# Kernel tuning notes

Measured on AMD Instinct MI355X. Metric: run time of the kernel, lower is better.

## Reference

```python
import jax, jax.numpy as jnp
import numpy as np

EPS = 1e-3  # tfa GroupNormalization default epsilon


def setup_inputs() -> dict:
    key = jax.random.key(0)
    ks = jax.random.split(key, 6)
    B, H, W, C = 8, 64, 64, 256
    x = jax.random.normal(ks[0], (B, H, W, C), dtype=jnp.float32)
    s = 0.05  # keep activations in a numerically sane range
    return {
        "x": x,
        "gamma": jnp.ones((C,), jnp.float32),
        "beta": jnp.zeros((C,), jnp.float32),
        "wq": jax.random.normal(ks[1], (C, C), jnp.float32) * s,
        "bq": jnp.zeros((C,), jnp.float32),
        "wk": jax.random.normal(ks[2], (C, C), jnp.float32) * s,
        "bk": jnp.zeros((C,), jnp.float32),
        "wv": jax.random.normal(ks[3], (C, C), jnp.float32) * s,
        "bv": jnp.zeros((C,), jnp.float32),
        "wp": jax.random.normal(ks[4], (C, C), jnp.float32) * s,
        "bp": jnp.zeros((C,), jnp.float32),
    }


def _group_norm1(x, gamma, beta):
    # GroupNorm with 1 group: normalize over (H, W, C) per sample,
    # per-channel affine. tfa default epsilon=1e-3.
    mean = jnp.mean(x, axis=(1, 2, 3), keepdims=True)
    var = jnp.var(x, axis=(1, 2, 3), keepdims=True)
    return (x - mean) * jax.lax.rsqrt(var + EPS) * gamma + beta


def reference(x, gamma, beta, wq, bq, wk, bk, wv, bv, wp, bp):
    B, H, W, C = x.shape
    h = _group_norm1(x, gamma, beta)
    hf = h.reshape(B, H * W, C)  # flatten spatial -> tokens
    q = hf @ wq + bq
    k = hf @ wk + bk
    v = hf @ wv + bv
    scale = jnp.float32(C) ** -0.5
    # full [B, N, N] attention scores, N = H*W (faithful to the einsum)
    scores = jnp.einsum('bnc,bmc->bnm', q, k) * scale
    attn = jax.nn.softmax(scores, axis=-1)
    o = jnp.einsum('bnm,bmc->bnc', attn, v)
    o = o @ wp + bp
    return x + o.reshape(B, H, W, C)
```

## Files before the change

kernel.cpp:

```cpp
#include <hip/hip_runtime.h>
#include <hip/hip_bf16.h>

typedef __attribute__((ext_vector_type(8))) short short8;
typedef __attribute__((ext_vector_type(4))) float f32x4;
typedef __attribute__((ext_vector_type(16))) float f32x16;
typedef long long ll_t;

#define WS_PART 0u
#define WS_STATS 4096u
#define WS_WT 8192u
#define WS_ML 532480u
#define WS_Q  2097152u
#define WS_K  (WS_Q + 16777216u)
#define WS_V  (WS_K + 16777216u)
#define WS_VT (WS_V + 16777216u)
#define WS_O  (WS_VT + 16777216u)

__device__ __forceinline__ unsigned short f2bf(float f) {
  unsigned int u = __builtin_bit_cast(unsigned int, f);
  u += 0x7fffu + ((u >> 16) & 1u);
  return (unsigned short)(u >> 16);
}
__device__ __forceinline__ float bf2f(unsigned short h) {
  unsigned int u = ((unsigned int)h) << 16;
  return __builtin_bit_cast(float, u);
}
__device__ __forceinline__ unsigned char f2fp8(float f) {
  return (unsigned char)(__builtin_amdgcn_cvt_pk_fp8_f32(f, f, 0, false) & 0xff);
}

__device__ __forceinline__ void gl_lds16(const unsigned short* g, unsigned short* l) {
  __builtin_amdgcn_global_load_lds(
      (const __attribute__((address_space(1))) unsigned int*)g,
      (__attribute__((address_space(3))) unsigned int*)l, 16, 0, 0);
}

__device__ __forceinline__ f32x4 mfma_fp8(ll_t a, ll_t b, f32x4 c) {
  return __builtin_amdgcn_mfma_f32_16x16x32_fp8_fp8(a, b, c, 0, 0, 0);
}

__global__ void k_wt(const float* __restrict__ wq, const float* __restrict__ wk,
                     const float* __restrict__ wv, const float* __restrict__ wp,
                     unsigned short* __restrict__ wT) {
  int m = blockIdx.x >> 8;
  int c = blockIdx.x & 255;
  const float* w = (m == 0) ? wq : (m == 1) ? wk : (m == 2) ? wv : wp;
  int d = threadIdx.x;
  wT[(size_t)(m * 256 + d) * 256 + c] = f2bf(w[c * 256 + d]);
}

__global__ void k_gn_part(const float* __restrict__ x, float2* __restrict__ part) {
  int b = blockIdx.x >> 5, seg = blockIdx.x & 31;
  const float4* xp = (const float4*)(x + ((size_t)b << 20) + ((size_t)seg << 15));
  float s = 0.f, sq = 0.f;
  for (int i = 0; i < 32; ++i) {
    float4 v = xp[threadIdx.x + i * 256];
    s += v.x + v.y + v.z + v.w;
    sq += v.x * v.x + v.y * v.y + v.z * v.z + v.w * v.w;
  }
  for (int m = 1; m <= 32; m <<= 1) { s += __shfl_xor(s, m); sq += __shfl_xor(sq, m); }
  __shared__ float2 red[4];
  int w = threadIdx.x >> 6;
  if ((threadIdx.x & 63) == 0) red[w] = make_float2(s, sq);
  __syncthreads();
  if (threadIdx.x == 0) {
    float S = 0.f, Q = 0.f;
    for (int i = 0; i < 4; ++i) { S += red[i].x; Q += red[i].y; }
    part[blockIdx.x] = make_float2(S, Q);
  }
}

__global__ void k_gn_stats(const float2* __restrict__ part, float2* __restrict__ stats) {
  int b = blockIdx.x, t = threadIdx.x;
  float s = 0.f, sq = 0.f;
  if (t < 32) { float2 p = part[b * 32 + t]; s = p.x; sq = p.y; }
  for (int m = 1; m <= 32; m <<= 1) { s += __shfl_xor(s, m); sq += __shfl_xor(sq, m); }
  if (t == 0) {
    float mean = s * (1.f / 1048576.f);
    float var = sq * (1.f / 1048576.f) - mean * mean;
    stats[b] = make_float2(mean, rsqrtf(var + 1e-3f));
  }
}

__global__ __launch_bounds__(256) void k_qkv(
    const float* __restrict__ x, const float* __restrict__ gamma, const float* __restrict__ beta,
    const float* __restrict__ bq, const float* __restrict__ bk, const float* __restrict__ bv,
    const float2* __restrict__ stats, const unsigned short* __restrict__ wT,
    unsigned char* __restrict__ q8, unsigned char* __restrict__ k8,
    unsigned char* __restrict__ vt8)
{
  __shared__ unsigned short SMEM[16384];
  unsigned short* const As = SMEM;
  unsigned short* const Bs = SMEM + 8192;
  const int bm = blockIdx.x, bn = blockIdx.y;
  const int mat = bn >> 1, dbase = (bn & 1) * 128;
  const int tid = threadIdx.x, lane = tid & 63, w = tid >> 6;
  const int wm = w >> 1, wn = w & 1;
  const int m0 = bm * 128;
  const float2 st = stats[bm >> 5];
  f32x16 acc[2][2] = {};
  for (int ks = 0; ks < 4; ++ks) {
    for (int i = 0; i < 8; ++i) {
      int chunk = tid + i * 256;
      int row = chunk >> 4, cq = (chunk & 15) * 4;
      int c = ks * 64 + cq;
      const float4 xv = *(const float4*)(x + (size_t)(m0 + row) * 256 + c);
      const float4 g = *(const float4*)(gamma + c);
      const float4 bt = *(const float4*)(beta + c);
      unsigned short h[4];
      h[0] = f2bf((xv.x - st.x) * st.y * g.x + bt.x);
      h[1] = f2bf((xv.y - st.x) * st.y * g.y + bt.y);
      h[2] = f2bf((xv.z - st.x) * st.y * g.z + bt.z);
      h[3] = f2bf((xv.w - st.x) * st.y * g.w + bt.w);
      *(uint2*)(&As[row * 64 + (cq ^ ((row & 7) << 3))]) = *(uint2*)h;
    }
    for (int i = 0; i < 4; ++i) {
      int chunk = tid + i * 256;
      int row = chunk >> 3, cc = (chunk & 7) * 8;
      const uint4* src = (const uint4*)(wT + (size_t)(mat * 256 + dbase + row) * 256 + ks * 64 + cc);
      *(uint4*)(&Bs[row * 64 + (cc ^ ((row & 7) << 3))]) = *src;
    }
    __syncthreads();
    for (int kk = 0; kk < 4; ++kk) {
      short8 a[2], b[2];
      for (int mi = 0; mi < 2; ++mi) {
        int row = wm * 64 + mi * 32 + (lane & 31);
        int off = (kk * 16 + (lane >> 5) * 8) ^ ((row & 7) << 3);
        a[mi] = *(const short8*)(&As[row * 64 + off]);
      }
      for (int ni = 0; ni < 2; ++ni) {
        int row = wn * 64 + ni * 32 + (lane & 31);
        int off = (kk * 16 + (lane >> 5) * 8) ^ ((row & 7) << 3);
        b[ni] = *(const short8*)(&Bs[row * 64 + off]);
      }
      for (int mi = 0; mi < 2; ++mi)
        for (int ni = 0; ni < 2; ++ni)
          acc[mi][ni] = __builtin_amdgcn_mfma_f32_32x32x16_bf16(a[mi], b[ni], acc[mi][ni], 0, 0, 0);
    }
    __syncthreads();
  }
  const int batch = bm >> 5;
  if (mat == 0) {
    for (int ni = 0; ni < 2; ++ni) {
      int dcol = dbase + wn * 64 + ni * 32 + (lane & 31);
      float bv_ = bq[dcol];
      for (int mi = 0; mi < 2; ++mi)
        for (int r = 0; r < 16; ++r) {
          int rowD = (r & 3) + 8 * (r >> 2) + 4 * (lane >> 5);
          int token = m0 + wm * 64 + mi * 32 + rowD;
          q8[(size_t)token * 256 + dcol] = f2fp8((acc[mi][ni][r] + bv_) * 0.25f);
        }
    }
  } else if (mat == 1) {
    for (int ni = 0; ni < 2; ++ni) {
      int dcol = dbase + wn * 64 + ni * 32 + (lane & 31);
      float bv_ = bk[dcol];
      size_t cbase = (size_t)(batch * 32 + (dcol >> 3)) * 32768 + (dcol & 7);
      for (int mi = 0; mi < 2; ++mi)
        for (int r = 0; r < 16; ++r) {
          int rowD = (r & 3) + 8 * (r >> 2) + 4 * (lane >> 5);
          int token = (m0 + wm * 64 + mi * 32 + rowD) & 4095;
          k8[cbase + (size_t)token * 8] = f2fp8((acc[mi][ni][r] + bv_) * 0.25f);
        }
    }
  } else {
    unsigned char* SB = (unsigned char*)SMEM;
    for (int ni = 0; ni < 2; ++ni) {
      int dloc = wn * 64 + ni * 32 + (lane & 31);
      float bv_ = bv[dbase + dloc];
      for (int mi = 0; mi < 2; ++mi)
        for (int r = 0; r < 16; ++r) {
          int tloc = wm * 64 + mi * 32 + (r & 3) + 8 * (r >> 2) + 4 * (lane >> 5);
          SB[dloc * 128 + (tloc ^ ((dloc & 7) << 4))] = f2fp8(acc[mi][ni][r] + bv_);
        }
    }
    __syncthreads();
    const int Tbase = (bm & 31) * 16;
    for (int i2 = 0; i2 < 4; ++i2) {
      int u = tid + i2 * 256;
      int T = u >> 6;
      int dp = u & 63;
      int d0 = dp * 2;
      int tb = T * 8;
      uint2 lo = *(const uint2*)(&SB[d0 * 128 + (tb ^ ((d0 & 7) << 4))]);
      uint2 hi2 = *(const uint2*)(&SB[(d0 + 1) * 128 + (tb ^ (((d0 + 1) & 7) << 4))]);
      uint4 vv = { lo.x, lo.y, hi2.x, hi2.y };
      *(uint4*)(vt8 + ((size_t)(batch * 512 + Tbase + T) * 256 + dbase + d0) * 8) = vv;
    }
  }
}

__global__ __launch_bounds__(512, 2) void k_attn(
    const unsigned char* __restrict__ q8, const unsigned char* __restrict__ k8,
    const unsigned char* __restrict__ vt8,
    unsigned short* __restrict__ part0, unsigned short* __restrict__ part1,
    float2* __restrict__ ml)
{
  __shared__ unsigned char LDSb[131072];
  unsigned char* const Ks0 = LDSb;
  unsigned char* const Ks1 = LDSb + 16384;
  unsigned char* const Vt0 = LDSb + 32768;
  unsigned char* const Vt1 = LDSb + 49152;
  const int g = blockIdx.x & 15, qt = blockIdx.x >> 4;
  const int batch = g >> 1, half = g & 1;
  const int q0 = qt * 256;
  const int tid = threadIdx.x, lane = tid & 63, li = lane & 15, hi = lane >> 4, w = tid >> 6;
  const float L2E = 1.44269504f;

  ll_t qf8[2][8];
#pragma unroll
  for (int qs = 0; qs < 2; ++qs) {
    const size_t qtok = (size_t)(batch * 4096 + q0 + w * 32 + qs * 16 + li);
#pragma unroll
    for (int kt = 0; kt < 8; ++kt)
      qf8[qs][kt] = *(const ll_t*)(q8 + qtok * 256 + kt * 32 + hi * 8);
  }
  f32x4 acc[2][16] = {};
  float m_r[2] = {-INFINITY, -INFINITY};
  float l_r[2] = {0.f, 0.f};
  const int idx0 = ((((hi << 1) + 0) & 3) * 16 + li) << 2;
  const int idx1 = ((((hi << 1) + 1) & 3) * 16 + li) << 2;

  unsigned kSrc[2];
  int kDst[2], vOff[2];
#pragma unroll
  for (int i = 0; i < 2; ++i) {
    kSrc[i] = (unsigned)((w * 4 + 2 * i + (lane >> 5)) * 32768 + (lane & 31) * 16);
    kDst[i] = (w * 4 + 2 * i) * 512 + lane * 16;
    vOff[i] = w * 2048 + i * 1024 + lane * 16;
  }
  const unsigned char* kb = k8 + (size_t)batch * 1048576 + half * 16384;
  const unsigned char* vb = vt8 + (size_t)batch * 1048576 + half * 524288;

#define STAGE(KD, VD) do {                                              \
    _Pragma("unroll")                                                   \
    for (int i = 0; i < 2; ++i)                                         \
      gl_lds16((const unsigned short*)(kb + kSrc[i]),                   \
               (unsigned short*)(KD + kDst[i]));                        \
    _Pragma("unroll")                                                   \
    for (int i = 0; i < 2; ++i)                                         \
      gl_lds16((const unsigned short*)(vb + vOff[i]),                   \
               (unsigned short*)(VD + vOff[i]));                        \
  } while (0)

#define QK(KVF, SDST, KC) do {                                               \
    _Pragma("unroll")                                                        \
    for (int ct = 0; ct < 2; ++ct)                                           \
      _Pragma("unroll")                                                      \
      for (int kt = 0; kt < 8; ++kt) {                                       \
        int boff = (((kt * 4 + hi) * 64) + (KVF) * 32 + ct * 16 + li) * 8;   \
        ll_t kf = *(const ll_t*)(&KC[boff]);                                 \
        SDST[0][ct] = mfma_fp8(kf, qf8[0][kt], SDST[0][ct]);                 \
        SDST[1][ct] = mfma_fp8(kf, qf8[1][kt], SDST[1][ct]);                 \
      }                                                                      \
  } while (0)

#define SOFTMAX(SARR, PF) do {                                               \
    float pm[2];                                                             \
    _Pragma("unroll")                                                        \
    for (int qs = 0; qs < 2; ++qs) {                                         \
      float p = fmaxf(fmaxf(fmaxf(SARR[qs][0][0], SARR[qs][0][1]),           \
                            fmaxf(SARR[qs][0][2], SARR[qs][0][3])),          \
                      fmaxf(fmaxf(SARR[qs][1][0], SARR[qs][1][1]),           \
                            fmaxf(SARR[qs][1][2], SARR[qs][1][3])));         \
      p = fmaxf(p, __shfl_xor(p, 16));                                       \
      p = fmaxf(p, __shfl_xor(p, 32));                                       \
      pm[qs] = p;                                                            \
    }                                                                        \
    if (!__all(fmaxf(pm[0] - m_r[0], pm[1] - m_r[1]) <= 4.0f)) {             \
      _Pragma("unroll")                                                      \
      for (int qs = 0; qs < 2; ++qs) {                                       \
        float mn = fmaxf(m_r[qs], pm[qs]);                                   \
        float corr = exp2f((m_r[qs] - mn) * L2E);                            \
        m_r[qs] = mn;                                                        \
        l_r[qs] *= corr;                                                     \
        float cq[4];                                                         \
        _Pragma("unroll")                                                    \
        for (int r = 0; r < 4; ++r) cq[r] = __shfl(corr, hi * 4 + r);        \
        _Pragma("unroll")                                                    \
        for (int dt = 0; dt < 16; ++dt)                                      \
          _Pragma("unroll")                                                  \
          for (int r = 0; r < 4; ++r) acc[qs][dt][r] *= cq[r];               \
      }                                                                      \
    }                                                                        \
    _Pragma("unroll")                                                        \
    for (int qs = 0; qs < 2; ++qs) {                                         \
      float rs = 0.f;                                                        \
      _Pragma("unroll")                                                      \
      for (int ct = 0; ct < 2; ++ct)                                         \
        _Pragma("unroll")                                                    \
        for (int r = 0; r < 4; ++r) {                                        \
          float p = exp2f((SARR[qs][ct][r] - m_r[qs]) * L2E);                \
          SARR[qs][ct][r] = p;                                               \
          rs += p;                                                           \
        }                                                                    \
      rs += __shfl_xor(rs, 16);                                              \
      rs += __shfl_xor(rs, 32);                                              \
      l_r[qs] += rs;                                                         \
      int D0 = __builtin_amdgcn_cvt_pk_fp8_f32(SARR[qs][0][0], SARR[qs][0][1], 0, false); \
      D0 = __builtin_amdgcn_cvt_pk_fp8_f32(SARR[qs][0][2], SARR[qs][0][3], D0, true);     \
      int D1 = __builtin_amdgcn_cvt_pk_fp8_f32(SARR[qs][1][0], SARR[qs][1][1], 0, false); \
      D1 = __builtin_amdgcn_cvt_pk_fp8_f32(SARR[qs][1][2], SARR[qs][1][3], D1, true);     \
      int a0 = __builtin_amdgcn_ds_bpermute(idx0, D0);                       \
      int a1 = __builtin_amdgcn_ds_bpermute(idx0, D1);                       \
      int b0 = __builtin_amdgcn_ds_bpermute(idx1, D0);                       \
      int b1 = __builtin_amdgcn_ds_bpermute(idx1, D1);                       \
      bool sel = (lane & 32) != 0;                                           \
      int2 pw = { sel ? a1 : a0, sel ? b1 : b0 };                            \
      PF[qs] = __builtin_bit_cast(ll_t, pw);                                 \
    }                                                                        \
  } while (0)

#define PV(KVF, PF, VC) do {                                                 \
    __builtin_amdgcn_s_setprio(1);                                          \
    _Pragma("unroll")                                                        \
    for (int dt = 0; dt < 16; ++dt) {                                        \
      int boff = ((((KVF) * 4 + hi) * 256) + dt * 16 + li) * 8;              \
      ll_t vf = *(const ll_t*)(&VC[boff]);                                   \
      acc[0][dt] = mfma_fp8(PF[0], vf, acc[0][dt]);                          \
      acc[1][dt] = mfma_fp8(PF[1], vf, acc[1][dt]);                          \
    }                                                                        \
    __builtin_amdgcn_s_setprio(0);                                          \
  } while (0)

  STAGE(Ks0, Vt0);
  for (int it = 0; it < 32; ++it) {
    const int cur = it & 1;
    __syncthreads();
    if (it < 31) {
      kb += 512;
      vb += 16384;
      if (cur) STAGE(Ks0, Vt0); else STAGE(Ks1, Vt1);
    }
    const unsigned char* Kc = cur ? Ks1 : Ks0;
    const unsigned char* Vc = cur ? Vt1 : Vt0;

    f32x4 s0[2][2] = {};
    __builtin_amdgcn_s_setprio(1);
    QK(0, s0, Kc);
    __builtin_amdgcn_s_setprio(0);
    ll_t pf0[2];
    SOFTMAX(s0, pf0);

    f32x4 s1[2][2] = {};
    __builtin_amdgcn_s_setprio(1);
    QK(1, s1, Kc);
    __builtin_amdgcn_s_setprio(0);
    PV(0, pf0, Vc);
    ll_t pf1[2];
    SOFTMAX(s1, pf1);
    PV(1, pf1, Vc);
  }
#undef STAGE
#undef QK
#undef SOFTMAX
#undef PV
  __syncthreads();
  if (lane < 16) {
#pragma unroll
    for (int qs = 0; qs < 2; ++qs)
      ml[half * 32768 + (size_t)batch * 4096 + q0 + w * 32 + qs * 16 + lane] =
          make_float2(m_r[qs], l_r[qs]);
  }
  unsigned short* Lw = (unsigned short*)LDSb + w * 8192;
#pragma unroll
  for (int qs = 0; qs < 2; ++qs)
#pragma unroll
    for (int dt = 0; dt < 16; ++dt)
#pragma unroll
      for (int r = 0; r < 4; ++r)
        Lw[(qs * 16 + hi * 4 + r) * 256 + dt * 16 + li] = f2bf(acc[qs][dt][r]);
  unsigned short* pout = (half ? part1 : part0) + ((size_t)batch * 4096 + q0 + w * 32) * 256;
#pragma unroll
  for (int i = 0; i < 16; ++i) {
    short8 v = *(const short8*)(&Lw[i * 512 + lane * 8]);
    int row = i * 2 + (lane >> 5);
    *(short8*)(pout + row * 256 + (lane & 31) * 8) = v;
  }
}

__global__ __launch_bounds__(256) void k_proj(
    const unsigned short* __restrict__ p0, const unsigned short* __restrict__ p1,
    const float2* __restrict__ ml, const unsigned short* __restrict__ wT,
    const float* __restrict__ bp, const float* __restrict__ x, float* __restrict__ out)
{
  __shared__ unsigned short As[128 * 64];
  __shared__ unsigned short Bs[128 * 64];
  const int bm = blockIdx.x, bn = blockIdx.y;
  const int dbase = bn * 128;
  const int tid = threadIdx.x, lane = tid & 63, w = tid >> 6;
  const int wm = w >> 1, wn = w & 1;
  const int m0 = bm * 128;
  f32x16 acc[2][2] = {};
  for (int ks = 0; ks < 4; ++ks) {
    for (int i = 0; i < 4; ++i) {
      int chunk = tid + i * 256;
      int row = chunk >> 3, cc = (chunk & 7) * 8;
      int tok = m0 + row;
      float2 a = ml[tok];
      float2 b2 = ml[32768 + tok];
      float mm = fmaxf(a.x, b2.x);
      float s0 = exp2f((a.x - mm) * 1.44269504f), s1 = exp2f((b2.x - mm) * 1.44269504f);
      float inv = 1.f / (s0 * a.y + s1 * b2.y);
      float r0 = s0 * inv, r1 = s1 * inv;
      short8 u0 = *(const short8*)(p0 + (size_t)tok * 256 + ks * 64 + cc);
      short8 u1 = *(const short8*)(p1 + (size_t)tok * 256 + ks * 64 + cc);
      unsigned short hh[8];
      for (int j = 0; j < 8; ++j)
        hh[j] = f2bf(r0 * bf2f((unsigned short)u0[j]) + r1 * bf2f((unsigned short)u1[j]));
      *(uint4*)(&As[row * 64 + (cc ^ ((row & 7) << 3))]) = *(uint4*)hh;
    }
    for (int i = 0; i < 4; ++i) {
      int chunk = tid + i * 256;
      int row = chunk >> 3, cc = (chunk & 7) * 8;
      const uint4* src = (const uint4*)(wT + (size_t)(3 * 256 + dbase + row) * 256 + ks * 64 + cc);
      *(uint4*)(&Bs[row * 64 + (cc ^ ((row & 7) << 3))]) = *src;
    }
    __syncthreads();
    for (int kk = 0; kk < 4; ++kk) {
      short8 a[2], b[2];
      for (int mi = 0; mi < 2; ++mi) {
        int row = wm * 64 + mi * 32 + (lane & 31);
        int off = (kk * 16 + (lane >> 5) * 8) ^ ((row & 7) << 3);
        a[mi] = *(const short8*)(&As[row * 64 + off]);
      }
      for (int ni = 0; ni < 2; ++ni) {
        int row = wn * 64 + ni * 32 + (lane & 31);
        int off = (kk * 16 + (lane >> 5) * 8) ^ ((row & 7) << 3);
        b[ni] = *(const short8*)(&Bs[row * 64 + off]);
      }
      for (int mi = 0; mi < 2; ++mi)
        for (int ni = 0; ni < 2; ++ni)
          acc[mi][ni] = __builtin_amdgcn_mfma_f32_32x32x16_bf16(a[mi], b[ni], acc[mi][ni], 0, 0, 0);
    }
    __syncthreads();
  }
  for (int ni = 0; ni < 2; ++ni) {
    int dcol = dbase + wn * 64 + ni * 32 + (lane & 31);
    float bv_ = bp[dcol];
    for (int mi = 0; mi < 2; ++mi)
      for (int r = 0; r < 16; ++r) {
        int rowD = (r & 3) + 8 * (r >> 2) + 4 * (lane >> 5);
        size_t idx = (size_t)(m0 + wm * 64 + mi * 32 + rowD) * 256 + dcol;
        out[idx] = x[idx] + acc[mi][ni][r] + bv_;
      }
  }
}

extern "C" void kernel_launch(void* const* d_in, const int* in_sizes, int n_in,
                              void* d_out, int out_size, void* d_ws, size_t ws_size,
                              hipStream_t stream) {
  const float* x = (const float*)d_in[0];
  const float* gamma = (const float*)d_in[1];
  const float* beta = (const float*)d_in[2];
  const float* wq = (const float*)d_in[3];
  const float* bq = (const float*)d_in[4];
  const float* wk = (const float*)d_in[5];
  const float* bk = (const float*)d_in[6];
  const float* wv = (const float*)d_in[7];
  const float* bv = (const float*)d_in[8];
  const float* wp = (const float*)d_in[9];
  const float* bp = (const float*)d_in[10];
  char* ws = (char*)d_ws;
  float2* part = (float2*)(ws + WS_PART);
  float2* stats = (float2*)(ws + WS_STATS);
  unsigned short* wT = (unsigned short*)(ws + WS_WT);
  float2* mlw = (float2*)(ws + WS_ML);
  unsigned char* q8 = (unsigned char*)(ws + WS_Q);
  unsigned char* k8 = (unsigned char*)(ws + WS_K);
  unsigned short* vw = (unsigned short*)(ws + WS_V);
  unsigned char* vt8 = (unsigned char*)(ws + WS_VT);
  unsigned short* ow = (unsigned short*)(ws + WS_O);
  float* out = (float*)d_out;

  k_wt<<<1024, 256, 0, stream>>>(wq, wk, wv, wp, wT);
  k_gn_part<<<256, 256, 0, stream>>>(x, part);
  k_gn_stats<<<8, 64, 0, stream>>>(part, stats);
  k_qkv<<<dim3(256, 6), 256, 0, stream>>>(x, gamma, beta, bq, bk, bv, stats, wT, q8, k8, vt8);
  k_attn<<<256, 512, 0, stream>>>(q8, k8, vt8, vw, ow, mlw);
  k_proj<<<dim3(256, 2), 256, 0, stream>>>(vw, ow, mlw, wT, bp, x, out);
}
```

Measured before the change: 205.3 us.

## Halve attention query tile per wave to double grid and raise occupancy

Each wave of the attention kernel now processes 16 query rows instead of 32. The grid doubles to 512 blocks and the LDS buffer shrinks to 64KB. The launch bound asks for 4 blocks per CU instead of 2, aiming for more resident waves and less register pressure. The cost is that every K/V tile staged into LDS now serves only half as many queries, so K/V global and LDS traffic per unit of work doubles. QK and PV are also serialized within each half-tile, which removes the previous overlap of PV(0) with QK(1).

Result: no change. 201.4 us (-1.9%).

```diff
diff --git a/kernel.cpp b/kernel.cpp
--- a/kernel.cpp
+++ b/kernel.cpp
@@ -190,34 +190,32 @@
   }
 }
 
-__global__ __launch_bounds__(512, 2) void k_attn(
+__global__ __launch_bounds__(512, 4) void k_attn(
     const unsigned char* __restrict__ q8, const unsigned char* __restrict__ k8,
     const unsigned char* __restrict__ vt8,
     unsigned short* __restrict__ part0, unsigned short* __restrict__ part1,
     float2* __restrict__ ml)
 {
-  __shared__ unsigned char LDSb[131072];
+  __shared__ unsigned char LDSb[65536];
   unsigned char* const Ks0 = LDSb;
   unsigned char* const Ks1 = LDSb + 16384;
   unsigned char* const Vt0 = LDSb + 32768;
   unsigned char* const Vt1 = LDSb + 49152;
   const int g = blockIdx.x & 15, qt = blockIdx.x >> 4;
   const int batch = g >> 1, half = g & 1;
-  const int q0 = qt * 256;
+  const int q0 = qt * 128;
   const int tid = threadIdx.x, lane = tid & 63, li = lane & 15, hi = lane >> 4, w = tid >> 6;
   const float L2E = 1.44269504f;
 
-  ll_t qf8[2][8];
-#pragma unroll
-  for (int qs = 0; qs < 2; ++qs) {
-    const size_t qtok = (size_t)(batch * 4096 + q0 + w * 32 + qs * 16 + li);
+  ll_t qf8[8];
+  {
+    const size_t qtok = (size_t)(batch * 4096 + q0 + w * 16 + li);
 #pragma unroll
     for (int kt = 0; kt < 8; ++kt)
-      qf8[qs][kt] = *(const ll_t*)(q8 + qtok * 256 + kt * 32 + hi * 8);
-  }
-  f32x4 acc[2][16] = {};
-  float m_r[2] = {-INFINITY, -INFINITY};
-  float l_r[2] = {0.f, 0.f};
+      qf8[kt] = *(const ll_t*)(q8 + qtok * 256 + kt * 32 + hi * 8);
+  }
+  f32x4 acc[16] = {};
+  float m_r = -INFINITY, l_r = 0.f;
   const int idx0 = ((((hi << 1) + 0) & 3) * 16 + li) << 2;
   const int idx1 = ((((hi << 1) + 1) & 3) * 16 + li) << 2;
 
@@ -250,65 +248,53 @@
       for (int kt = 0; kt < 8; ++kt) {                                       \
         int boff = (((kt * 4 + hi) * 64) + (KVF) * 32 + ct * 16 + li) * 8;   \
         ll_t kf = *(const ll_t*)(&KC[boff]);                                 \
-        SDST[0][ct] = mfma_fp8(kf, qf8[0][kt], SDST[0][ct]);                 \
-        SDST[1][ct] = mfma_fp8(kf, qf8[1][kt], SDST[1][ct]);                 \
+        SDST[ct] = mfma_fp8(kf, qf8[kt], SDST[ct]);                          \
       }                                                                      \
   } while (0)
 
 #define SOFTMAX(SARR, PF) do {                                               \
-    float pm[2];                                                             \
+    float pm = fmaxf(fmaxf(fmaxf(SARR[0][0], SARR[0][1]),                    \
+                           fmaxf(SARR[0][2], SARR[0][3])),                   \
+                     fmaxf(fmaxf(SARR[1][0], SARR[1][1]),                    \
+                           fmaxf(SARR[1][2], SARR[1][3])));                  \
+    pm = fmaxf(pm, __shfl_xor(pm, 16));                                      \
+    pm = fmaxf(pm, __shfl_xor(pm, 32));                                      \
+    if (!__all(pm - m_r <= 4.0f)) {                                          \
+      float mn = fmaxf(m_r, pm);                                             \
+      float corr = exp2f((m_r - mn) * L2E);                                  \
+      m_r = mn;                                                              \
+      l_r *= corr;                                                           \
+      float cq[4];                                                           \
+      _Pragma("unroll")                                                      \
+      for (int r = 0; r < 4; ++r) cq[r] = __shfl(corr, hi * 4 + r);          \
+      _Pragma("unroll")                                                      \
+      for (int dt = 0; dt < 16; ++dt)                                        \
+        _Pragma("unroll")                                                    \
+        for (int r = 0; r < 4; ++r) acc[dt][r] *= cq[r];                     \
+    }                                                                        \
+    float rs = 0.f;                                                          \
     _Pragma("unroll")                                                        \
-    for (int qs = 0; qs < 2; ++qs) {                                         \
-      float p = fmaxf(fmaxf(fmaxf(SARR[qs][0][0], SARR[qs][0][1]),           \
-                            fmaxf(SARR[qs][0][2], SARR[qs][0][3])),          \
-                      fmaxf(fmaxf(SARR[qs][1][0], SARR[qs][1][1]),           \
-                            fmaxf(SARR[qs][1][2], SARR[qs][1][3])));         \
-      p = fmaxf(p, __shfl_xor(p, 16));                                       \
-      p = fmaxf(p, __shfl_xor(p, 32));                                       \
-      pm[qs] = p;                                                            \
-    }                                                                        \
-    if (!__all(fmaxf(pm[0] - m_r[0], pm[1] - m_r[1]) <= 4.0f)) {             \
+    for (int ct = 0; ct < 2; ++ct)                                           \
       _Pragma("unroll")                                                      \
-      for (int qs = 0; qs < 2; ++qs) {                                       \
-        float mn = fmaxf(m_r[qs], pm[qs]);                                   \
-        float corr = exp2f((m_r[qs] - mn) * L2E);                            \
-        m_r[qs] = mn;                                                        \
-        l_r[qs] *= corr;                                                     \
-        float cq[4];                                                         \
-        _Pragma("unroll")                                                    \
-        for (int r = 0; r < 4; ++r) cq[r] = __shfl(corr, hi * 4 + r);        \
-        _Pragma("unroll")                                                    \
-        for (int dt = 0; dt < 16; ++dt)                                      \
-          _Pragma("unroll")                                                  \
-          for (int r = 0; r < 4; ++r) acc[qs][dt][r] *= cq[r];               \
+      for (int r = 0; r < 4; ++r) {                                          \
+        float p = exp2f((SARR[ct][r] - m_r) * L2E);                          \
+        SARR[ct][r] = p;                                                     \
+        rs += p;                                                             \
       }                                                                      \
-    }                                                                        \
-    _Pragma("unroll")                                                        \
-    for (int qs = 0; qs < 2; ++qs) {                                         \
-      float rs = 0.f;                                                        \
-      _Pragma("unroll")                                                      \
-      for (int ct = 0; ct < 2; ++ct)                                         \
-        _Pragma("unroll")                                                    \
-        for (int r = 0; r < 4; ++r) {                                        \
-          float p = exp2f((SARR[qs][ct][r] - m_r[qs]) * L2E);                \
-          SARR[qs][ct][r] = p;                                               \
-          rs += p;                                                           \
-        }                                                                    \
-      rs += __shfl_xor(rs, 16);                                              \
-      rs += __shfl_xor(rs, 32);                                              \
-      l_r[qs] += rs;                                                         \
-      int D0 = __builtin_amdgcn_cvt_pk_fp8_f32(SARR[qs][0][0], SARR[qs][0][1], 0, false); \
-      D0 = __builtin_amdgcn_cvt_pk_fp8_f32(SARR[qs][0][2], SARR[qs][0][3], D0, true);     \
-      int D1 = __builtin_amdgcn_cvt_pk_fp8_f32(SARR[qs][1][0], SARR[qs][1][1], 0, false); \
-      D1 = __builtin_amdgcn_cvt_pk_fp8_f32(SARR[qs][1][2], SARR[qs][1][3], D1, true);     \
-      int a0 = __builtin_amdgcn_ds_bpermute(idx0, D0);                       \
-      int a1 = __builtin_amdgcn_ds_bpermute(idx0, D1);                       \
-      int b0 = __builtin_amdgcn_ds_bpermute(idx1, D0);                       \
-      int b1 = __builtin_amdgcn_ds_bpermute(idx1, D1);                       \
-      bool sel = (lane & 32) != 0;                                           \
-      int2 pw = { sel ? a1 : a0, sel ? b1 : b0 };                            \
-      PF[qs] = __builtin_bit_cast(ll_t, pw);                                 \
-    }                                                                        \
+    rs += __shfl_xor(rs, 16);                                                \
+    rs += __shfl_xor(rs, 32);                                                \
+    l_r += rs;                                                               \
+    int D0 = __builtin_amdgcn_cvt_pk_fp8_f32(SARR[0][0], SARR[0][1], 0, false); \
+    D0 = __builtin_amdgcn_cvt_pk_fp8_f32(SARR[0][2], SARR[0][3], D0, true);     \
+    int D1 = __builtin_amdgcn_cvt_pk_fp8_f32(SARR[1][0], SARR[1][1], 0, false); \
+    D1 = __builtin_amdgcn_cvt_pk_fp8_f32(SARR[1][2], SARR[1][3], D1, true);     \
+    int a0 = __builtin_amdgcn_ds_bpermute(idx0, D0);                         \
+    int a1 = __builtin_amdgcn_ds_bpermute(idx0, D1);                         \
+    int b0 = __builtin_amdgcn_ds_bpermute(idx1, D0);                         \
+    int b1 = __builtin_amdgcn_ds_bpermute(idx1, D1);                         \
+    bool sel = (lane & 32) != 0;                                             \
+    int2 pw = { sel ? a1 : a0, sel ? b1 : b0 };                              \
+    PF = __builtin_bit_cast(ll_t, pw);                                       \
   } while (0)
 
 #define PV(KVF, PF, VC) do {                                                 \
@@ -317,8 +303,7 @@
     for (int dt = 0; dt < 16; ++dt) {                                        \
       int boff = ((((KVF) * 4 + hi) * 256) + dt * 16 + li) * 8;              \
       ll_t vf = *(const ll_t*)(&VC[boff]);                                   \
-      acc[0][dt] = mfma_fp8(PF[0], vf, acc[0][dt]);                          \
-      acc[1][dt] = mfma_fp8(PF[1], vf, acc[1][dt]);                          \
+      acc[dt] = mfma_fp8(PF, vf, acc[dt]);                                   \
     }                                                                        \
     __builtin_amdgcn_s_setprio(0);                                          \
   } while (0)
@@ -335,44 +320,41 @@
     const unsigned char* Kc = cur ? Ks1 : Ks0;
     const unsigned char* Vc = cur ? Vt1 : Vt0;
 
-    f32x4 s0[2][2] = {};
-    __builtin_amdgcn_s_setprio(1);
-    QK(0, s0, Kc);
-    __builtin_amdgcn_s_setprio(0);
-    ll_t pf0[2];
-    SOFTMAX(s0, pf0);
-
-    f32x4 s1[2][2] = {};
-    __builtin_amdgcn_s_setprio(1);
-    QK(1, s1, Kc);
-    __builtin_amdgcn_s_setprio(0);
-    PV(0, pf0, Vc);
-    ll_t pf1[2];
-    SOFTMAX(s1, pf1);
-    PV(1, pf1, Vc);
+    {
+      f32x4 s0[2] = {};
+      __builtin_amdgcn_s_setprio(1);
+      QK(0, s0, Kc);
+      __builtin_amdgcn_s_setprio(0);
+      ll_t pf0;
+      SOFTMAX(s0, pf0);
+      PV(0, pf0, Vc);
+    }
+    {
+      f32x4 s1[2] = {};
+      __builtin_amdgcn_s_setprio(1);
+      QK(1, s1, Kc);
+      __builtin_amdgcn_s_setprio(0);
+      ll_t pf1;
+      SOFTMAX(s1, pf1);
+      PV(1, pf1, Vc);
+    }
   }
 #undef STAGE
 #undef QK
 #undef SOFTMAX
 #undef PV
   __syncthreads();
-  if (lane < 16) {
+  if (lane < 16)
+    ml[half * 32768 + (size_t)batch * 4096 + q0 + w * 16 + lane] = make_float2(m_r, l_r);
+  unsigned short* Lw = (unsigned short*)LDSb + w * 4096;
 #pragma unroll
-    for (int qs = 0; qs < 2; ++qs)
-      ml[half * 32768 + (size_t)batch * 4096 + q0 + w * 32 + qs * 16 + lane] =
-          make_float2(m_r[qs], l_r[qs]);
-  }
-  unsigned short* Lw = (unsigned short*)LDSb + w * 8192;
+  for (int dt = 0; dt < 16; ++dt)
 #pragma unroll
-  for (int qs = 0; qs < 2; ++qs)
+    for (int r = 0; r < 4; ++r)
+      Lw[(hi * 4 + r) * 256 + dt * 16 + li] = f2bf(acc[dt][r]);
+  unsigned short* pout = (half ? part1 : part0) + ((size_t)batch * 4096 + q0 + w * 16) * 256;
 #pragma unroll
-    for (int dt = 0; dt < 16; ++dt)
-#pragma unroll
-      for (int r = 0; r < 4; ++r)
-        Lw[(qs * 16 + hi * 4 + r) * 256 + dt * 16 + li] = f2bf(acc[qs][dt][r]);
-  unsigned short* pout = (half ? part1 : part0) + ((size_t)batch * 4096 + q0 + w * 32) * 256;
-#pragma unroll
-  for (int i = 0; i < 16; ++i) {
+  for (int i = 0; i < 8; ++i) {
     short8 v = *(const short8*)(&Lw[i * 512 + lane * 8]);
     int row = i * 2 + (lane >> 5);
     *(short8*)(pout + row * 256 + (lane & 31) * 8) = v;
@@ -477,6 +459,6 @@
   k_gn_part<<<256, 256, 0, stream>>>(x, part);
   k_gn_stats<<<8, 64, 0, stream>>>(part, stats);
   k_qkv<<<dim3(256, 6), 256, 0, stream>>>(x, gamma, beta, bq, bk, bv, stats, wT, q8, k8, vt8);
-  k_attn<<<256, 512, 0, stream>>>(q8, k8, vt8, vw, ow, mlw);
+  k_attn<<<512, 512, 0, stream>>>(q8, k8, vt8, vw, ow, mlw);
   k_proj<<<dim3(256, 2), 256, 0, stream>>>(vw, ow, mlw, wT, bp, x, out);
 }
```
